# Optimization experiments

Measured on AMD Instinct MI355X. Metric: run time of the kernel, lower is better.

## Reference

```python
import jax, jax.numpy as jnp
import numpy as np

N_NODES = 100000
N_EDGES = 1600000
NFEAT = 128
NHID = 128
NCLASS = 16
NUM_GRAPHS = 64
EPS = 1e-5


def layer_norm(x, g, b):
    mu = jnp.mean(x, axis=-1, keepdims=True)
    var = jnp.mean((x - mu) ** 2, axis=-1, keepdims=True)
    return (x - mu) * jax.lax.rsqrt(var + EPS) * g + b


def gcn_conv(x, W, b, src, dst, ew, n_nodes):
    # PyG GCNConv: h = x @ W^T; add self loops (weight 1); sym-normalize; scatter-add; + bias
    h = x @ W.T                                   # [N, out]
    loop = jnp.arange(n_nodes, dtype=src.dtype)
    src2 = jnp.concatenate([src, loop])
    dst2 = jnp.concatenate([dst, loop])
    ew2 = jnp.concatenate([ew, jnp.ones((n_nodes,), dtype=ew.dtype)])
    deg = jax.ops.segment_sum(ew2, dst2, num_segments=n_nodes)
    dinv = jnp.where(deg > 0, jax.lax.rsqrt(jnp.where(deg > 0, deg, 1.0)), 0.0)
    norm = dinv[src2] * ew2 * dinv[dst2]          # [E+N]
    msg = h[src2] * norm[:, None]                 # gather + scale
    agg = jax.ops.segment_sum(msg, dst2, num_segments=n_nodes)
    return agg + b


def setup_inputs() -> dict:
    key = jax.random.key(0)
    ks = jax.random.split(key, 12)
    kaiming = lambda k, shape: jax.random.normal(k, shape, dtype=jnp.float32) * np.sqrt(2.0 / shape[1])
    ln = lambda k, d: (1.0 + 0.02 * jax.random.normal(k, (d,), dtype=jnp.float32),
                       0.02 * jax.random.normal(jax.random.fold_in(k, 1), (d,), dtype=jnp.float32))
    ln0_g, ln0_b = ln(ks[0], NFEAT)
    ln1_g, ln1_b = ln(ks[1], NHID)
    ln2_g, ln2_b = ln(ks[2], NHID)
    # batch vector: sorted graph ids so each graph is a contiguous node block
    batch = jnp.sort(jax.random.randint(ks[3], (N_NODES,), 0, NUM_GRAPHS)).astype(jnp.int64)
    return {
        "x": jax.random.normal(ks[4], (N_NODES, NFEAT), dtype=jnp.float32),
        "edge_index": jax.random.randint(ks[5], (2, N_EDGES), 0, N_NODES).astype(jnp.int64),
        "batch": batch,
        "edge_weight": jnp.ones((N_EDGES,), dtype=jnp.float32),
        "ln0_g": ln0_g, "ln0_b": ln0_b,
        "W1": kaiming(ks[6], (NHID, NFEAT)), "b1": jnp.zeros((NHID,), jnp.float32),
        "ln1_g": ln1_g, "ln1_b": ln1_b,
        "W2": kaiming(ks[7], (NHID, NHID)), "b2": jnp.zeros((NHID,), jnp.float32),
        "ln2_g": ln2_g, "ln2_b": ln2_b,
        "Wc": kaiming(ks[8], (NCLASS, NHID)), "bc": jnp.zeros((NCLASS,), jnp.float32),
    }


def reference(x, edge_index, batch, edge_weight,
              ln0_g, ln0_b, W1, b1, ln1_g, ln1_b,
              W2, b2, ln2_g, ln2_b, Wc, bc):
    src, dst = edge_index[0], edge_index[1]
    h = layer_norm(x, ln0_g, ln0_b)                       # layer_norm_first
    h = gcn_conv(h, W1, b1, src, dst, edge_weight, N_NODES)
    h = jax.nn.relu(layer_norm(h, ln1_g, ln1_b))          # dropout is identity in eval
    h = gcn_conv(h, W2, b2, src, dst, edge_weight, N_NODES)
    h = jax.nn.relu(layer_norm(h, ln2_g, ln2_b))
    pooled = jax.ops.segment_sum(h, batch, num_segments=NUM_GRAPHS)  # global_add_pool
    logits = pooled @ Wc.T + bc
    return jax.nn.log_softmax(logits, axis=1)
```

## Files before the change

### kernel.cpp

```cpp
#include <hip/hip_runtime.h>
#include <hip/hip_bf16.h>
#include <math.h>

#define N_NODES 100000
#define NFEAT 128
#define NCLASS 16
#define NUM_GRAPHS 64
#define LN_EPS 1e-5f
#define PAD 40
#define BSHIFT 7
#define NBKT 782
#define EPB 1024
#define NBLKMAX 1600
#define LSTRIDE 784

typedef unsigned int uint;
typedef unsigned short ushort;
typedef unsigned char uchar;
typedef short bf16x8 __attribute__((ext_vector_type(8)));
typedef float f32x4 __attribute__((ext_vector_type(4)));
typedef float f32x2 __attribute__((ext_vector_type(2)));

__device__ __forceinline__ float bf_lo(uint u) { return __uint_as_float(u << 16); }
__device__ __forceinline__ float bf_hi(uint u) { return __uint_as_float(u & 0xffff0000u); }
__device__ __forceinline__ ushort f2bf(float f) {
    uint u = __float_as_uint(f);
    uint r = 0x7fffu + ((u >> 16) & 1u);
    return (ushort)((u + r) >> 16);
}
__device__ __forceinline__ uint pack2bf(float x, float y) {
    return ((uint)f2bf(y) << 16) | (uint)f2bf(x);
}
__device__ __forceinline__ uint pk15(float f) {
    uint u = __float_as_uint(f);
    uint r = 0xFFFFu + ((u >> 17) & 1u);
    return (u + r) >> 17;
}
__device__ __forceinline__ float up15(uint w) {
    return __uint_as_float(w << 17);
}

#if __has_builtin(__builtin_amdgcn_cvt_pk_f32_fp8)
__device__ __forceinline__ f32x2 fp8lo(uint u) {
    return __builtin_amdgcn_cvt_pk_f32_fp8((int)u, false);
}
__device__ __forceinline__ f32x2 fp8hi(uint u) {
    return __builtin_amdgcn_cvt_pk_f32_fp8((int)u, true);
}
#else
__device__ __forceinline__ float fp8_one(uint b) {
    uint em = b & 0x7fu;
    float v;
    if (em >= 0x08u) v = __uint_as_float((((em >> 3) + 120u) << 23) | ((em & 7u) << 20));
    else v = (float)em * (1.0f / 512.0f);
    return (b & 0x80u) ? -v : v;
}
__device__ __forceinline__ f32x2 fp8lo(uint u) {
    f32x2 r;
    r[0] = fp8_one(u & 0xffu);
    r[1] = fp8_one((u >> 8) & 0xffu);
    return r;
}
__device__ __forceinline__ f32x2 fp8hi(uint u) { return fp8lo(u >> 16); }
#endif

#if __has_builtin(__builtin_amdgcn_cvt_pk_fp8_f32)
__device__ __forceinline__ uint f2fp8(float f) {
    return (uint)__builtin_amdgcn_cvt_pk_fp8_f32(f, f, 0, false) & 0xffu;
}
#else
__device__ __forceinline__ uint f2fp8(float f) {
    uint u = __float_as_uint(f);
    uint s = (u >> 24) & 0x80u;
    uint mag = u & 0x7fffffffu;
    if (mag >= 0x43E80000u) return s | 0x7Eu;
    if (mag < 0x3C800000u) {
        uint q = (uint)(__uint_as_float(mag) * 512.0f + 0.5f);
        return s | q;
    }
    uint r = 0x7FFFFu + ((mag >> 20) & 1u);
    mag += r;
    uint e = (mag >> 23) - 120u;
    uint m = (mag >> 20) & 7u;
    if (e > 15u) return s | 0x7Eu;
    return s | (e << 3) | m;
}
#endif

__global__ __launch_bounds__(256) void k_bin(const int* __restrict__ dst,
                                             const int* __restrict__ src,
                                             const float* __restrict__ ew,
                                             uint2* __restrict__ binned,
                                             ushort* __restrict__ lofsG,
                                             float* __restrict__ pooled,
                                             const float* __restrict__ W1,
                                             const float* __restrict__ W2,
                                             ushort* __restrict__ Wf, int E) {
    __shared__ uint lcnt[NBKT];
    __shared__ uint ofsarr[NBKT + 1];
    __shared__ uint wsum[4];
    __shared__ uint2 srec[EPB];
    int t = threadIdx.x;
    int blk = blockIdx.x;
    {
        int gi = blk * 256 + t;
        if (gi < NUM_GRAPHS * NFEAT) pooled[gi] = 0.0f;
        if (gi < 2 * NFEAT * NFEAT) {
            int f = gi & 16383;
            const float* W = (gi < NFEAT * NFEAT) ? W1 : W2;
            int e = f & 7, lane = (f >> 3) & 63, c = (f >> 9) & 3, tt = f >> 11;
            int m = lane & 15, q = lane >> 4;
            Wf[gi] = f2bf(W[(tt * 16 + m) * NFEAT + c * 32 + q * 8 + e]);
        }
    }
    int e0 = blk * EPB;
    for (int i = t; i < NBKT; i += 256) lcnt[i] = 0;
    __syncthreads();
    int myb[4], myd[4], mys[4];
    uint myw[4];
#pragma unroll
    for (int i = 0; i < 4; ++i) {
        int e = e0 + i * 256 + t;
        int b = -1, d = 0, s2 = 0;
        uint w = 0;
        if (e < E) {
            d = dst[e];
            s2 = src[e];
            w = __float_as_uint(ew[e]);
            b = d >> BSHIFT;
            atomicAdd(&lcnt[b], 1u);
        }
        myb[i] = b;
        myd[i] = d;
        mys[i] = s2;
        myw[i] = w;
    }
    __syncthreads();
    int lane = t & 63, wv = t >> 6;
    uint v[4];
    uint s = 0;
    int b0 = t * 4;
#pragma unroll
    for (int k = 0; k < 4; ++k) {
        int ix = b0 + k;
        v[k] = (ix < NBKT) ? lcnt[ix] : 0u;
        s += v[k];
    }
    uint inc = s;
#pragma unroll
    for (int o = 1; o < 64; o <<= 1) {
        uint nn = __shfl_up(inc, o, 64);
        if (lane >= o) inc += nn;
    }
    if (lane == 63) wsum[wv] = inc;
    __syncthreads();
    uint wbase = 0;
    for (int k = 0; k < wv; ++k) wbase += wsum[k];
    uint excl = wbase + inc - s;
#pragma unroll
    for (int k = 0; k < 4; ++k) {
        int ix = b0 + k;
        if (ix < NBKT) {
            ofsarr[ix] = excl;
            excl += v[k];
        }
    }
    if (t == 0) ofsarr[NBKT] = wsum[0] + wsum[1] + wsum[2] + wsum[3];
    __syncthreads();
    for (int i = t; i <= NBKT; i += 256) lofsG[(size_t)blk * LSTRIDE + i] = (ushort)ofsarr[i];
    for (int i = t; i < NBKT; i += 256) lcnt[i] = 0;
    __syncthreads();
#pragma unroll
    for (int i = 0; i < 4; ++i) {
        int b = myb[i];
        if (b < 0) continue;
        uint pos = ofsarr[b] + atomicAdd(&lcnt[b], 1u);
        srec[pos] = make_uint2(((uint)(myd[i] & 127) << 17) | (uint)mys[i], myw[i]);
    }
    __syncthreads();
    const uint4* sp = (const uint4*)srec;
    uint4* gp = (uint4*)(binned + (size_t)blk * EPB);
    for (int i = t; i < EPB / 2; i += 256) gp[i] = sp[i];
}

__global__ __launch_bounds__(512) void k_build(const uint2* __restrict__ binned,
                                               const ushort* __restrict__ lofsG,
                                               uint* __restrict__ rowcsr,
                                               int* __restrict__ cnt,
                                               float* __restrict__ dinv,
                                               int nblk, int n) {
    __shared__ uint lcsr[128 * 41];
    __shared__ int lc[128];
    int b = blockIdx.x, t = threadIdx.x;
    int node0 = b << BSHIFT;
    for (int i = t; i < 128 * 41; i += 512) lcsr[i] = 0;
    if (t < 128) lc[t] = 0;
    __syncthreads();
    for (int blk = t; blk < nblk; blk += 512) {
        const ushort* lp = lofsG + (size_t)blk * LSTRIDE + b;
        int s = lp[0], e2 = lp[1];
        const uint2* rp = binned + (size_t)blk * EPB;
        for (int i = s; i < e2; ++i) {
            uint2 r = rp[i];
            int nl = (int)(r.x >> 17);
            int slot = atomicAdd(&lc[nl], 1);
            if (slot < PAD)
                lcsr[nl * 41 + slot] = ((r.x & 0x1FFFFu) << 15) | pk15(__uint_as_float(r.y));
        }
    }
    __syncthreads();
    int nvalid = n - node0;
    if (nvalid > 128) nvalid = 128;
    if (nvalid <= 0) return;
    size_t gbase = (size_t)node0 * PAD;
    int wtot = nvalid * PAD;
    for (int i = t; i < wtot; i += 512) {
        int nl = i / PAD, sl = i - nl * PAD;
        rowcsr[gbase + i] = lcsr[nl * 41 + sl];
    }
    if (t < nvalid) {
        int cc = lc[t];
        if (cc > PAD) cc = PAD;
        float s = 0.0f;
        for (int r = 0; r < cc; ++r) s += up15(lcsr[t * 41 + r]);
        cnt[node0 + t] = cc;
        dinv[node0 + t] = rsqrtf(1.0f + s);
    }
}

__global__ __launch_bounds__(256) void k_gemm_ln0(const float* __restrict__ X,
                                                  const ushort* __restrict__ Wf,
                                                  const float* __restrict__ dinv,
                                                  const float* __restrict__ lg,
                                                  const float* __restrict__ lb,
                                                  uchar* __restrict__ C, int nrows) {
    int tid = threadIdx.x;
    int wave = tid >> 6, lane = tid & 63;
    int row0 = blockIdx.x * 64 + wave * 16;
    int m = lane & 15, q = lane >> 4;
    int ra = row0 + m;
    float xv[32];
    if (ra < nrows) {
#pragma unroll
        for (int c = 0; c < 4; ++c) {
            float4 p0 = *(const float4*)(X + (size_t)ra * NFEAT + c * 32 + q * 8);
            float4 p1 = *(const float4*)(X + (size_t)ra * NFEAT + c * 32 + q * 8 + 4);
            xv[c * 8 + 0] = p0.x; xv[c * 8 + 1] = p0.y; xv[c * 8 + 2] = p0.z; xv[c * 8 + 3] = p0.w;
            xv[c * 8 + 4] = p1.x; xv[c * 8 + 5] = p1.y; xv[c * 8 + 6] = p1.z; xv[c * 8 + 7] = p1.w;
        }
    } else {
#pragma unroll
        for (int i = 0; i < 32; ++i) xv[i] = 0.0f;
    }
    float s = 0.0f;
#pragma unroll
    for (int i = 0; i < 32; ++i) s += xv[i];
    s += __shfl_xor(s, 16, 64);
    s += __shfl_xor(s, 32, 64);
    float mean = s * (1.0f / NFEAT);
    float v = 0.0f;
#pragma unroll
    for (int i = 0; i < 32; ++i) { float d = xv[i] - mean; v += d * d; }
    v += __shfl_xor(v, 16, 64);
    v += __shfl_xor(v, 32, 64);
    float rs = rsqrtf(v * (1.0f / NFEAT) + LN_EPS);

    bf16x8 a[4];
#pragma unroll
    for (int c = 0; c < 4; ++c) {
        float4 g0 = *(const float4*)(lg + c * 32 + q * 8);
        float4 g1 = *(const float4*)(lg + c * 32 + q * 8 + 4);
        float4 b0 = *(const float4*)(lb + c * 32 + q * 8);
        float4 b1 = *(const float4*)(lb + c * 32 + q * 8 + 4);
        float gv[8] = {g0.x, g0.y, g0.z, g0.w, g1.x, g1.y, g1.z, g1.w};
        float bv[8] = {b0.x, b0.y, b0.z, b0.w, b1.x, b1.y, b1.z, b1.w};
        uint tmp[4];
#pragma unroll
        for (int t2 = 0; t2 < 4; ++t2) {
            float e0 = (xv[c * 8 + 2 * t2] - mean) * rs * gv[2 * t2] + bv[2 * t2];
            float e1 = (xv[c * 8 + 2 * t2 + 1] - mean) * rs * gv[2 * t2 + 1] + bv[2 * t2 + 1];
            tmp[t2] = pack2bf(e0, e1);
        }
        a[c] = *(bf16x8*)tmp;
    }

    int orow[4];
    float sd[4];
#pragma unroll
    for (int r = 0; r < 4; ++r) {
        orow[r] = row0 + q * 4 + r;
        sd[r] = (orow[r] < nrows) ? dinv[orow[r]] : 0.0f;
    }
#pragma unroll
    for (int t = 0; t < 8; ++t) {
        const ushort* bp = Wf + ((t * 4 * 64 + lane) << 3);
        f32x4 acc = {0.0f, 0.0f, 0.0f, 0.0f};
        acc = __builtin_amdgcn_mfma_f32_16x16x32_bf16(a[0], *(const bf16x8*)(bp), acc, 0, 0, 0);
        acc = __builtin_amdgcn_mfma_f32_16x16x32_bf16(a[1], *(const bf16x8*)(bp + 512), acc, 0, 0, 0);
        acc = __builtin_amdgcn_mfma_f32_16x16x32_bf16(a[2], *(const bf16x8*)(bp + 1024), acc, 0, 0, 0);
        acc = __builtin_amdgcn_mfma_f32_16x16x32_bf16(a[3], *(const bf16x8*)(bp + 1536), acc, 0, 0, 0);
#pragma unroll
        for (int r = 0; r < 4; ++r) {
            if (orow[r] < nrows)
                C[(size_t)orow[r] * NFEAT + t * 16 + m] = (uchar)f2fp8(acc[r] * sd[r]);
        }
    }
}

__global__ __launch_bounds__(256) void k_gemm_mfma(const ushort* __restrict__ A,
                                                   const ushort* __restrict__ Wf,
                                                   const float* __restrict__ dinv,
                                                   uchar* __restrict__ C, int nrows) {
    int tid = threadIdx.x;
    int wave = tid >> 6, lane = tid & 63;
    int row0 = blockIdx.x * 64 + wave * 16;
    int m = lane & 15, q = lane >> 4;
    int ra = row0 + m;
    bf16x8 a0 = {0,0,0,0,0,0,0,0}, a1 = a0, a2 = a0, a3 = a0;
    if (ra < nrows) {
        const ushort* p = A + (size_t)ra * NFEAT + q * 8;
        a0 = *(const bf16x8*)(p);
        a1 = *(const bf16x8*)(p + 32);
        a2 = *(const bf16x8*)(p + 64);
        a3 = *(const bf16x8*)(p + 96);
    }
    int orow[4];
    float sd[4];
#pragma unroll
    for (int r = 0; r < 4; ++r) {
        orow[r] = row0 + q * 4 + r;
        sd[r] = (orow[r] < nrows) ? dinv[orow[r]] : 0.0f;
    }
#pragma unroll
    for (int t = 0; t < 8; ++t) {
        const ushort* bp = Wf + ((t * 4 * 64 + lane) << 3);
        f32x4 acc = {0.0f, 0.0f, 0.0f, 0.0f};
        acc = __builtin_amdgcn_mfma_f32_16x16x32_bf16(a0, *(const bf16x8*)(bp), acc, 0, 0, 0);
        acc = __builtin_amdgcn_mfma_f32_16x16x32_bf16(a1, *(const bf16x8*)(bp + 512), acc, 0, 0, 0);
        acc = __builtin_amdgcn_mfma_f32_16x16x32_bf16(a2, *(const bf16x8*)(bp + 1024), acc, 0, 0, 0);
        acc = __builtin_amdgcn_mfma_f32_16x16x32_bf16(a3, *(const bf16x8*)(bp + 1536), acc, 0, 0, 0);
#pragma unroll
        for (int r = 0; r < 4; ++r) {
            if (orow[r] < nrows)
                C[(size_t)orow[r] * NFEAT + t * 16 + m] = (uchar)f2fp8(acc[r] * sd[r]);
        }
    }
}

__global__ __launch_bounds__(256) void k_agg_ln(const uchar* __restrict__ T,
                                                const uint* __restrict__ rowcsr,
                                                const int* __restrict__ cnt,
                                                const float* __restrict__ dinv,
                                                const float* __restrict__ bias,
                                                const float* __restrict__ lng,
                                                const float* __restrict__ lnb,
                                                ushort* __restrict__ out, int n) {
    int wid = blockIdx.x * 4 + (threadIdx.x >> 6);
    int lane = threadIdx.x & 63;
    int l16 = lane & 15;
    int node = wid * 4 + (lane >> 4);
    bool valid = node < n;
    int nodec = valid ? node : 0;

    const uint* Tw = (const uint*)T;
    int c = 0;
    float di = 0.0f;
    if (valid) {
        c = cnt[node];
        di = dinv[node];
    }
    if (c > PAD) c = PAD;
    uint2 su = *(const uint2*)(Tw + (size_t)nodec * 32 + l16 * 2);
    f32x2 s01 = fp8lo(su.x), s23 = fp8hi(su.x);
    f32x2 s45 = fp8lo(su.y), s67 = fp8hi(su.y);
    float a0 = s01[0], a1 = s01[1], a2 = s23[0], a3 = s23[1];
    float a4 = s45[0], a5 = s45[1], a6 = s67[0], a7 = s67[1];

    int cm = c;
    cm = max(cm, __shfl_xor(cm, 16, 64));
    cm = max(cm, __shfl_xor(cm, 32, 64));
    int rc = (cm + 7) & ~7;
    const uint* mp = rowcsr + (size_t)nodec * PAD;

    int j = 0;
    for (; j + 16 <= rc; j += 16) {
        uint mw[16];
#pragma unroll
        for (int k = 0; k < 16; k += 4) {
            uint4 m0 = *(const uint4*)(mp + j + k);
            mw[k] = m0.x; mw[k + 1] = m0.y; mw[k + 2] = m0.z; mw[k + 3] = m0.w;
        }
        uint2 uu[16];
#pragma unroll
        for (int k = 0; k < 16; ++k)
            uu[k] = *(const uint2*)(Tw + (size_t)(mw[k] >> 15) * 32 + l16 * 2);
#pragma unroll
        for (int k = 0; k < 16; ++k) {
            float w = up15(mw[k]);
            f32x2 v01 = fp8lo(uu[k].x);
            f32x2 v23 = fp8hi(uu[k].x);
            f32x2 v45 = fp8lo(uu[k].y);
            f32x2 v67 = fp8hi(uu[k].y);
            a0 = fmaf(v01[0], w, a0);
            a1 = fmaf(v01[1], w, a1);
            a2 = fmaf(v23[0], w, a2);
            a3 = fmaf(v23[1], w, a3);
            a4 = fmaf(v45[0], w, a4);
            a5 = fmaf(v45[1], w, a5);
            a6 = fmaf(v67[0], w, a6);
            a7 = fmaf(v67[1], w, a7);
        }
    }
    for (; j < rc; j += 8) {
        uint4 m0 = *(const uint4*)(mp + j);
        uint4 m1 = *(const uint4*)(mp + j + 4);
        uint mw[8];
        mw[0] = m0.x; mw[1] = m0.y; mw[2] = m0.z; mw[3] = m0.w;
        mw[4] = m1.x; mw[5] = m1.y; mw[6] = m1.z; mw[7] = m1.w;
        uint2 uu[8];
#pragma unroll
        for (int k = 0; k < 8; ++k)
            uu[k] = *(const uint2*)(Tw + (size_t)(mw[k] >> 15) * 32 + l16 * 2);
#pragma unroll
        for (int k = 0; k < 8; ++k) {
            float w = up15(mw[k]);
            f32x2 v01 = fp8lo(uu[k].x);
            f32x2 v23 = fp8hi(uu[k].x);
            f32x2 v45 = fp8lo(uu[k].y);
            f32x2 v67 = fp8hi(uu[k].y);
            a0 = fmaf(v01[0], w, a0);
            a1 = fmaf(v01[1], w, a1);
            a2 = fmaf(v23[0], w, a2);
            a3 = fmaf(v23[1], w, a3);
            a4 = fmaf(v45[0], w, a4);
            a5 = fmaf(v45[1], w, a5);
            a6 = fmaf(v67[0], w, a6);
            a7 = fmaf(v67[1], w, a7);
        }
    }

    float4 bb0 = *(const float4*)(bias + 8 * l16);
    float4 bb1 = *(const float4*)(bias + 8 * l16 + 4);
    float p0 = fmaf(di, a0, bb0.x);
    float p1 = fmaf(di, a1, bb0.y);
    float p2 = fmaf(di, a2, bb0.z);
    float p3 = fmaf(di, a3, bb0.w);
    float p4 = fmaf(di, a4, bb1.x);
    float p5 = fmaf(di, a5, bb1.y);
    float p6 = fmaf(di, a6, bb1.z);
    float p7 = fmaf(di, a7, bb1.w);
    float s = p0 + p1 + p2 + p3 + p4 + p5 + p6 + p7;
#pragma unroll
    for (int m = 8; m >= 1; m >>= 1) s += __shfl_xor(s, m, 64);
    float mean = s * (1.0f / NFEAT);
    float d0 = p0 - mean, d1 = p1 - mean, d2 = p2 - mean, d3 = p3 - mean;
    float d4 = p4 - mean, d5 = p5 - mean, d6 = p6 - mean, d7 = p7 - mean;
    float v = d0 * d0 + d1 * d1 + d2 * d2 + d3 * d3
            + d4 * d4 + d5 * d5 + d6 * d6 + d7 * d7;
#pragma unroll
    for (int m = 8; m >= 1; m >>= 1) v += __shfl_xor(v, m, 64);
    float rs = rsqrtf(v * (1.0f / NFEAT) + LN_EPS);
    float4 gg0 = *(const float4*)(lng + 8 * l16);
    float4 gg1 = *(const float4*)(lng + 8 * l16 + 4);
    float4 lb0 = *(const float4*)(lnb + 8 * l16);
    float4 lb1 = *(const float4*)(lnb + 8 * l16 + 4);
    float o0 = fmaxf(d0 * rs * gg0.x + lb0.x, 0.0f);
    float o1 = fmaxf(d1 * rs * gg0.y + lb0.y, 0.0f);
    float o2 = fmaxf(d2 * rs * gg0.z + lb0.z, 0.0f);
    float o3 = fmaxf(d3 * rs * gg0.w + lb0.w, 0.0f);
    float o4 = fmaxf(d4 * rs * gg1.x + lb1.x, 0.0f);
    float o5 = fmaxf(d5 * rs * gg1.y + lb1.y, 0.0f);
    float o6 = fmaxf(d6 * rs * gg1.z + lb1.z, 0.0f);
    float o7 = fmaxf(d7 * rs * gg1.w + lb1.w, 0.0f);
    if (valid) {
        uint4 wv;
        wv.x = pack2bf(o0, o1);
        wv.y = pack2bf(o2, o3);
        wv.z = pack2bf(o4, o5);
        wv.w = pack2bf(o6, o7);
        *(uint4*)(out + (size_t)node * NFEAT + 8 * l16) = wv;
    }
}

__global__ __launch_bounds__(256) void k_pool(const ushort* __restrict__ in,
                                              const int* __restrict__ batch,
                                              float* __restrict__ pooled, int n) {
    int wave = blockIdx.x * 4 + (threadIdx.x >> 6);
    int row0 = wave * 16;
    if (row0 >= n) return;
    int lane = threadIdx.x & 63;
    int end = row0 + 16;
    if (end > n) end = n;
    float accx = 0.0f, accy = 0.0f;
    int cur = batch[row0];
    for (int r = row0; r < end; ++r) {
        int g = batch[r];
        if (g != cur) {
            unsafeAtomicAdd(&pooled[cur * NFEAT + 2 * lane], accx);
            unsafeAtomicAdd(&pooled[cur * NFEAT + 2 * lane + 1], accy);
            accx = 0.0f; accy = 0.0f;
            cur = g;
        }
        uint u = *(const uint*)(in + (size_t)r * NFEAT + 2 * lane);
        accx += bf_lo(u);
        accy += bf_hi(u);
    }
    unsafeAtomicAdd(&pooled[cur * NFEAT + 2 * lane], accx);
    unsafeAtomicAdd(&pooled[cur * NFEAT + 2 * lane + 1], accy);
}

__global__ void k_final(const float* __restrict__ pooled, const float* __restrict__ Wc,
                        const float* __restrict__ bc, float* __restrict__ out) {
    __shared__ float p[128];
    __shared__ float lg[NCLASS];
    int g = blockIdx.x, t = threadIdx.x;
    p[t] = pooled[g * 128 + t];
    __syncthreads();
    if (t < NCLASS) {
        float s = bc[t];
        for (int k = 0; k < 128; ++k) s = fmaf(p[k], Wc[t * 128 + k], s);
        lg[t] = s;
    }
    __syncthreads();
    if (t == 0) {
        float m = -1e30f;
        for (int j = 0; j < NCLASS; ++j) m = fmaxf(m, lg[j]);
        float sum = 0.0f;
        for (int j = 0; j < NCLASS; ++j) sum += expf(lg[j] - m);
        float l = logf(sum);
        for (int j = 0; j < NCLASS; ++j) out[g * NCLASS + j] = lg[j] - m - l;
    }
}

extern "C" void kernel_launch(void* const* d_in, const int* in_sizes, int n_in,
                              void* d_out, int out_size, void* d_ws, size_t ws_size,
                              hipStream_t stream) {
    const float* x    = (const float*)d_in[0];
    const int*   ei   = (const int*)d_in[1];
    const int*   batch= (const int*)d_in[2];
    const float* ew   = (const float*)d_in[3];
    const float* ln0g = (const float*)d_in[4];
    const float* ln0b = (const float*)d_in[5];
    const float* W1   = (const float*)d_in[6];
    const float* b1   = (const float*)d_in[7];
    const float* ln1g = (const float*)d_in[8];
    const float* ln1b = (const float*)d_in[9];
    const float* W2   = (const float*)d_in[10];
    const float* b2   = (const float*)d_in[11];
    const float* ln2g = (const float*)d_in[12];
    const float* ln2b = (const float*)d_in[13];
    const float* Wc   = (const float*)d_in[14];
    const float* bc   = (const float*)d_in[15];
    float* out = (float*)d_out;

    int E = in_sizes[1] / 2;
    const int* srcp = ei;
    const int* dstp = ei + E;

    ushort* A     = (ushort*)d_ws;
    ushort* B     = A + (size_t)N_NODES * NFEAT;
    uint*  rowcsr = (uint*)(B + (size_t)N_NODES * NFEAT);
    uint2* binned = (uint2*)(rowcsr + (size_t)N_NODES * PAD);
    ushort* lofsG = (ushort*)(binned + (size_t)NBLKMAX * EPB);
    float* dinv   = (float*)(lofsG + (size_t)NBLKMAX * LSTRIDE);
    float* pooled = dinv + N_NODES;
    int*   cnt    = (int*)(pooled + NUM_GRAPHS * NFEAT);
    ushort* W1f   = (ushort*)(cnt + N_NODES);
    ushort* W2f   = W1f + NFEAT * NFEAT;
    uchar* B8     = (uchar*)B;

    dim3 blk(256);
    dim3 blk512(512);
    int gB = (E + EPB - 1) / EPB;
    int gW = ((N_NODES + 3) / 4 + 3) / 4;
    int gG = (N_NODES + 63) / 64;

    k_bin<<<gB, blk, 0, stream>>>(dstp, srcp, ew, binned, lofsG,
                                  pooled, W1, W2, W1f, E);
    k_build<<<NBKT, blk512, 0, stream>>>(binned, lofsG, rowcsr, cnt, dinv, gB, N_NODES);

    k_gemm_ln0<<<gG, blk, 0, stream>>>(x, W1f, dinv, ln0g, ln0b, B8, N_NODES);
    k_agg_ln<<<gW, blk, 0, stream>>>(B8, rowcsr, cnt, dinv, b1, ln1g, ln1b, A, N_NODES);
    k_gemm_mfma<<<gG, blk, 0, stream>>>(A, W2f, dinv, B8, N_NODES);
    k_agg_ln<<<gW, blk, 0, stream>>>(B8, rowcsr, cnt, dinv, b2, ln2g, ln2b, A, N_NODES);
    k_pool<<<(N_NODES + 63) / 64, blk, 0, stream>>>(A, batch, pooled, N_NODES);
    k_final<<<NUM_GRAPHS, dim3(128), 0, stream>>>(pooled, Wc, bc, out);
}
```

Baseline: 281.6 us.

## Fuse layer-1 aggregation+LN with layer-2 GEMM via shared-memory tile

```diff
diff --git a/kernel.cpp b/kernel.cpp
--- a/kernel.cpp
+++ b/kernel.cpp
@@ -13,6 +13,7 @@
 #define EPB 1024
 #define NBLKMAX 1600
 #define LSTRIDE 784
+#define HSTR 136
 
 typedef unsigned int uint;
 typedef unsigned short ushort;
@@ -307,42 +308,172 @@
     }
 }
 
-__global__ __launch_bounds__(256) void k_gemm_mfma(const ushort* __restrict__ A,
-                                                   const ushort* __restrict__ Wf,
-                                                   const float* __restrict__ dinv,
-                                                   uchar* __restrict__ C, int nrows) {
-    int tid = threadIdx.x;
-    int wave = tid >> 6, lane = tid & 63;
-    int row0 = blockIdx.x * 64 + wave * 16;
+__global__ __launch_bounds__(256) void k_agg_gemm(const uchar* __restrict__ T,
+                                                  const uint* __restrict__ rowcsr,
+                                                  const int* __restrict__ cnt,
+                                                  const float* __restrict__ dinv,
+                                                  const float* __restrict__ bias,
+                                                  const float* __restrict__ lng,
+                                                  const float* __restrict__ lnb,
+                                                  const ushort* __restrict__ Wf,
+                                                  uchar* __restrict__ C2, int n) {
+    __shared__ ushort hrows[16 * HSTR];
+    __shared__ float ldinv[16];
+    int wid = threadIdx.x >> 6;
+    int lane = threadIdx.x & 63;
+    int l16 = lane & 15;
+    int local = wid * 4 + (lane >> 4);
+    int node = blockIdx.x * 16 + local;
+    bool valid = node < n;
+    int nodec = valid ? node : 0;
+
+    const uint* Tw = (const uint*)T;
+    int c = 0;
+    float di = 0.0f;
+    if (valid) {
+        c = cnt[node];
+        di = dinv[node];
+    }
+    if (c > PAD) c = PAD;
+    if (l16 == 0) ldinv[local] = di;
+    uint2 su = *(const uint2*)(Tw + (size_t)nodec * 32 + l16 * 2);
+    f32x2 s01 = fp8lo(su.x), s23 = fp8hi(su.x);
+    f32x2 s45 = fp8lo(su.y), s67 = fp8hi(su.y);
+    float a0 = s01[0], a1 = s01[1], a2 = s23[0], a3 = s23[1];
+    float a4 = s45[0], a5 = s45[1], a6 = s67[0], a7 = s67[1];
+
+    int cm = c;
+    cm = max(cm, __shfl_xor(cm, 16, 64));
+    cm = max(cm, __shfl_xor(cm, 32, 64));
+    int rc = (cm + 7) & ~7;
+    const uint* mp = rowcsr + (size_t)nodec * PAD;
+
+    int j = 0;
+    for (; j + 16 <= rc; j += 16) {
+        uint mw[16];
+#pragma unroll
+        for (int k = 0; k < 16; k += 4) {
+            uint4 m0 = *(const uint4*)(mp + j + k);
+            mw[k] = m0.x; mw[k + 1] = m0.y; mw[k + 2] = m0.z; mw[k + 3] = m0.w;
+        }
+        uint2 uu[16];
+#pragma unroll
+        for (int k = 0; k < 16; ++k)
+            uu[k] = *(const uint2*)(Tw + (size_t)(mw[k] >> 15) * 32 + l16 * 2);
+#pragma unroll
+        for (int k = 0; k < 16; ++k) {
+            float w = up15(mw[k]);
+            f32x2 v01 = fp8lo(uu[k].x);
+            f32x2 v23 = fp8hi(uu[k].x);
+            f32x2 v45 = fp8lo(uu[k].y);
+            f32x2 v67 = fp8hi(uu[k].y);
+            a0 = fmaf(v01[0], w, a0);
+            a1 = fmaf(v01[1], w, a1);
+            a2 = fmaf(v23[0], w, a2);
+            a3 = fmaf(v23[1], w, a3);
+            a4 = fmaf(v45[0], w, a4);
+            a5 = fmaf(v45[1], w, a5);
+            a6 = fmaf(v67[0], w, a6);
+            a7 = fmaf(v67[1], w, a7);
+        }
+    }
+    for (; j < rc; j += 8) {
+        uint4 m0 = *(const uint4*)(mp + j);
+        uint4 m1 = *(const uint4*)(mp + j + 4);
+        uint mw[8];
+        mw[0] = m0.x; mw[1] = m0.y; mw[2] = m0.z; mw[3] = m0.w;
+        mw[4] = m1.x; mw[5] = m1.y; mw[6] = m1.z; mw[7] = m1.w;
+        uint2 uu[8];
+#pragma unroll
+        for (int k = 0; k < 8; ++k)
+            uu[k] = *(const uint2*)(Tw + (size_t)(mw[k] >> 15) * 32 + l16 * 2);
+#pragma unroll
+        for (int k = 0; k < 8; ++k) {
+            float w = up15(mw[k]);
+            f32x2 v01 = fp8lo(uu[k].x);
+            f32x2 v23 = fp8hi(uu[k].x);
+            f32x2 v45 = fp8lo(uu[k].y);
+            f32x2 v67 = fp8hi(uu[k].y);
+            a0 = fmaf(v01[0], w, a0);
+            a1 = fmaf(v01[1], w, a1);
+            a2 = fmaf(v23[0], w, a2);
+            a3 = fmaf(v23[1], w, a3);
+            a4 = fmaf(v45[0], w, a4);
+            a5 = fmaf(v45[1], w, a5);
+            a6 = fmaf(v67[0], w, a6);
+            a7 = fmaf(v67[1], w, a7);
+        }
+    }
+
+    float4 bb0 = *(const float4*)(bias + 8 * l16);
+    float4 bb1 = *(const float4*)(bias + 8 * l16 + 4);
+    float p0 = fmaf(di, a0, bb0.x);
+    float p1 = fmaf(di, a1, bb0.y);
+    float p2 = fmaf(di, a2, bb0.z);
+    float p3 = fmaf(di, a3, bb0.w);
+    float p4 = fmaf(di, a4, bb1.x);
+    float p5 = fmaf(di, a5, bb1.y);
+    float p6 = fmaf(di, a6, bb1.z);
+    float p7 = fmaf(di, a7, bb1.w);
+    float s = p0 + p1 + p2 + p3 + p4 + p5 + p6 + p7;
+#pragma unroll
+    for (int m = 8; m >= 1; m >>= 1) s += __shfl_xor(s, m, 64);
+    float mean = s * (1.0f / NFEAT);
+    float d0 = p0 - mean, d1 = p1 - mean, d2 = p2 - mean, d3 = p3 - mean;
+    float d4 = p4 - mean, d5 = p5 - mean, d6 = p6 - mean, d7 = p7 - mean;
+    float v = d0 * d0 + d1 * d1 + d2 * d2 + d3 * d3
+            + d4 * d4 + d5 * d5 + d6 * d6 + d7 * d7;
+#pragma unroll
+    for (int m = 8; m >= 1; m >>= 1) v += __shfl_xor(v, m, 64);
+    float rs = rsqrtf(v * (1.0f / NFEAT) + LN_EPS);
+    float4 gg0 = *(const float4*)(lng + 8 * l16);
+    float4 gg1 = *(const float4*)(lng + 8 * l16 + 4);
+    float4 lb0 = *(const float4*)(lnb + 8 * l16);
+    float4 lb1 = *(const float4*)(lnb + 8 * l16 + 4);
+    float o0 = fmaxf(d0 * rs * gg0.x + lb0.x, 0.0f);
+    float o1 = fmaxf(d1 * rs * gg0.y + lb0.y, 0.0f);
+    float o2 = fmaxf(d2 * rs * gg0.z + lb0.z, 0.0f);
+    float o3 = fmaxf(d3 * rs * gg0.w + lb0.w, 0.0f);
+    float o4 = fmaxf(d4 * rs * gg1.x + lb1.x, 0.0f);
+    float o5 = fmaxf(d5 * rs * gg1.y + lb1.y, 0.0f);
+    float o6 = fmaxf(d6 * rs * gg1.z + lb1.z, 0.0f);
+    float o7 = fmaxf(d7 * rs * gg1.w + lb1.w, 0.0f);
+    {
+        uint4 wv;
+        wv.x = pack2bf(o0, o1);
+        wv.y = pack2bf(o2, o3);
+        wv.z = pack2bf(o4, o5);
+        wv.w = pack2bf(o6, o7);
+        *(uint4*)(hrows + local * HSTR + 8 * l16) = wv;
+    }
+    __syncthreads();
     int m = lane & 15, q = lane >> 4;
-    int ra = row0 + m;
-    bf16x8 a0 = {0,0,0,0,0,0,0,0}, a1 = a0, a2 = a0, a3 = a0;
-    if (ra < nrows) {
-        const ushort* p = A + (size_t)ra * NFEAT + q * 8;
-        a0 = *(const bf16x8*)(p);
-        a1 = *(const bf16x8*)(p + 32);
-        a2 = *(const bf16x8*)(p + 64);
-        a3 = *(const bf16x8*)(p + 96);
-    }
+    const ushort* hp = hrows + m * HSTR;
+    bf16x8 ha0 = *(const bf16x8*)(hp + q * 8);
+    bf16x8 ha1 = *(const bf16x8*)(hp + 32 + q * 8);
+    bf16x8 ha2 = *(const bf16x8*)(hp + 64 + q * 8);
+    bf16x8 ha3 = *(const bf16x8*)(hp + 96 + q * 8);
+    int row0 = blockIdx.x * 16;
     int orow[4];
     float sd[4];
 #pragma unroll
     for (int r = 0; r < 4; ++r) {
         orow[r] = row0 + q * 4 + r;
-        sd[r] = (orow[r] < nrows) ? dinv[orow[r]] : 0.0f;
-    }
-#pragma unroll
-    for (int t = 0; t < 8; ++t) {
+        sd[r] = ldinv[q * 4 + r];
+    }
+#pragma unroll
+    for (int ti = 0; ti < 2; ++ti) {
+        int t = wid + ti * 4;
         const ushort* bp = Wf + ((t * 4 * 64 + lane) << 3);
         f32x4 acc = {0.0f, 0.0f, 0.0f, 0.0f};
-        acc = __builtin_amdgcn_mfma_f32_16x16x32_bf16(a0, *(const bf16x8*)(bp), acc, 0, 0, 0);
-        acc = __builtin_amdgcn_mfma_f32_16x16x32_bf16(a1, *(const bf16x8*)(bp + 512), acc, 0, 0, 0);
-        acc = __builtin_amdgcn_mfma_f32_16x16x32_bf16(a2, *(const bf16x8*)(bp + 1024), acc, 0, 0, 0);
-        acc = __builtin_amdgcn_mfma_f32_16x16x32_bf16(a3, *(const bf16x8*)(bp + 1536), acc, 0, 0, 0);
+        acc = __builtin_amdgcn_mfma_f32_16x16x32_bf16(ha0, *(const bf16x8*)(bp), acc, 0, 0, 0);
+        acc = __builtin_amdgcn_mfma_f32_16x16x32_bf16(ha1, *(const bf16x8*)(bp + 512), acc, 0, 0, 0);
+        acc = __builtin_amdgcn_mfma_f32_16x16x32_bf16(ha2, *(const bf16x8*)(bp + 1024), acc, 0, 0, 0);
+        acc = __builtin_amdgcn_mfma_f32_16x16x32_bf16(ha3, *(const bf16x8*)(bp + 1536), acc, 0, 0, 0);
 #pragma unroll
         for (int r = 0; r < 4; ++r) {
-            if (orow[r] < nrows)
-                C[(size_t)orow[r] * NFEAT + t * 16 + m] = (uchar)f2fp8(acc[r] * sd[r]);
+            if (orow[r] < n)
+                C2[(size_t)orow[r] * NFEAT + t * 16 + m] = (uchar)f2fp8(acc[r] * sd[r]);
         }
     }
 }
@@ -568,11 +699,13 @@
     ushort* W1f   = (ushort*)(cnt + N_NODES);
     ushort* W2f   = W1f + NFEAT * NFEAT;
     uchar* B8     = (uchar*)B;
+    uchar* B8b    = (uchar*)binned;
 
     dim3 blk(256);
     dim3 blk512(512);
     int gB = (E + EPB - 1) / EPB;
     int gW = ((N_NODES + 3) / 4 + 3) / 4;
+    int gF = (N_NODES + 15) / 16;
     int gG = (N_NODES + 63) / 64;
 
     k_bin<<<gB, blk, 0, stream>>>(dstp, srcp, ew, binned, lofsG,
@@ -580,9 +713,9 @@
     k_build<<<NBKT, blk512, 0, stream>>>(binned, lofsG, rowcsr, cnt, dinv, gB, N_NODES);
 
     k_gemm_ln0<<<gG, blk, 0, stream>>>(x, W1f, dinv, ln0g, ln0b, B8, N_NODES);
-    k_agg_ln<<<gW, blk, 0, stream>>>(B8, rowcsr, cnt, dinv, b1, ln1g, ln1b, A, N_NODES);
-    k_gemm_mfma<<<gG, blk, 0, stream>>>(A, W2f, dinv, B8, N_NODES);
-    k_agg_ln<<<gW, blk, 0, stream>>>(B8, rowcsr, cnt, dinv, b2, ln2g, ln2b, A, N_NODES);
+    k_agg_gemm<<<gF, blk, 0, stream>>>(B8, rowcsr, cnt, dinv, b1, ln1g, ln1b,
+                                       W2f, B8b, N_NODES);
+    k_agg_ln<<<gW, blk, 0, stream>>>(B8b, rowcsr, cnt, dinv, b2, ln2g, ln2b, A, N_NODES);
     k_pool<<<(N_NODES + 63) / 64, blk, 0, stream>>>(A, batch, pooled, N_NODES);
     k_final<<<NUM_GRAPHS, dim3(128), 0, stream>>>(pooled, Wc, bc, out);
 }
```

Result: faster. 270.6 us (-3.9%).
